# Optimization experiments

Measured on AMD Instinct MI355X. Metric: run time of the kernel, lower is better.

The kernel has to match this reference:

```python
import jax, jax.numpy as jnp
import numpy as np

B, L, K, E, D, H = 16, 512, 48, 128, 384, 128

def _gelu(x):
    return jax.nn.gelu(x, approximate=False)  # torch nn.GELU default is erf-based

def setup_inputs() -> dict:
    key = jax.random.key(0)
    ks = jax.random.split(key, 16)
    def randn(k, shape, scale=1.0):
        return jax.random.normal(k, shape, dtype=jnp.float32) * scale
    inp = {
        "h_V": randn(ks[0], (B, L, D)),
        "h_E": randn(ks[1], (B, L, K, E)),
        "mask": jnp.ones((B, L), dtype=jnp.float32),
        "fw1": randn(ks[2], (E, D), 1.0 / np.sqrt(E)),
        "fb1": randn(ks[3], (D,), 0.02),
        "fw2": randn(ks[4], (D, D), 1.0 / np.sqrt(D)),
        "fb2": randn(ks[5], (D,), 0.02),
        "hw1": randn(ks[6], (D, H), 1.0 / np.sqrt(D)),
        "hb1": randn(ks[7], (H,), 0.02),
        "hw2": randn(ks[8], (H, H // 2), 1.0 / np.sqrt(H)),
        "hb2": randn(ks[9], (H // 2,), 0.02),
        "hw3": randn(ks[10], (H // 2, 1), 1.0 / np.sqrt(H // 2)),
        "hb3": randn(ks[11], (1,), 0.02),
        "E_idx": jax.random.randint(ks[12], (B, L, K), 0, L),
    }
    return inp

def reference(h_V, h_E, mask, fw1, fb1, fw2, fb2, hw1, hb1, hw2, hb2, hw3, hb3, E_idx):
    # CFConv: edge-conditioned filters [B,L,K,D]
    W = _gelu(_gelu(h_E @ fw1 + fb1) @ fw2 + fb2)
    # gather_nodes: x_j[b,l,k,:] = h_V[b, E_idx[b,l,k], :]
    x_j = jax.vmap(lambda x, idx: x[idx])(h_V, E_idx)  # [B,L,K,D]
    h = jnp.sum(x_j * W, axis=2)  # weighted sum over neighbors -> [B,L,D]
    # mlp_head (dropout = identity at inference)
    h = _gelu(h @ hw1 + hb1)
    h = _gelu(h @ hw2 + hb2)
    dG = (h @ hw3 + hb3)[..., 0]  # [B,L]
    valid_length = jnp.clip(jnp.sum(mask, axis=1), 1.0, None)  # [B]
    return jnp.sum(dG * mask, axis=1) / jnp.sqrt(valid_length)  # [B]
```

## Files before the change

kernel.cpp:

```cpp
#include <hip/hip_runtime.h>
#include <hip/hip_bf16.h>
#include <math.h>

#define NB 16
#define NL 512
#define NK 48
#define NE 128
#define ND 384
#define NH 128

typedef __attribute__((ext_vector_type(8))) short short8;
typedef __attribute__((ext_vector_type(4))) float f32x4;

__device__ __forceinline__ float gelu_fast(float x) {
    float t = x * fmaf(x * x, -0.1029437f, -2.3022087f);
    float e = __builtin_amdgcn_exp2f(t);
    return x * __builtin_amdgcn_rcpf(1.0f + e);
}

__device__ __forceinline__ unsigned short f2bf(float x) {
    union { float f; unsigned u; } v; v.f = x;
    unsigned r = v.u + 0x7fffu + ((v.u >> 16) & 1u);
    return (unsigned short)(r >> 16);
}

__device__ __forceinline__ unsigned short f2bf_rhu(float x) {
    union { float f; unsigned u; } v; v.f = x;
    return (unsigned short)((v.u + 0x8000u) >> 16);
}

__device__ __forceinline__ unsigned pk_bf16(float a, float b) {
    union { float f; unsigned u; } ua, ub; ua.f = a; ub.f = b;
    return __builtin_amdgcn_perm(ua.u + 0x8000u, ub.u + 0x8000u, 0x07060302u);
}

__global__ void pack_weights(const float* __restrict__ fw1,
                             const float* __restrict__ fw2,
                             const float* __restrict__ hw1,
                             const float* __restrict__ hw2,
                             unsigned short* __restrict__ fw1p,
                             unsigned short* __restrict__ fw2p,
                             unsigned short* __restrict__ hw1p,
                             unsigned short* __restrict__ hw2p,
                             float* __restrict__ dGsum) {
    int tid = blockIdx.x * 256 + threadIdx.x;
    if (tid < NB) dGsum[tid] = 0.0f;
    if (tid < NE * ND) {
        int k = tid / ND, n = tid % ND;
        int dst = (((k >> 5) * 24 + (n >> 4)) * 64 + ((k >> 3) & 3) * 16 + (n & 15)) * 8 + (k & 7);
        fw1p[dst] = f2bf(fw1[tid]);
    } else if (tid < NE * ND + ND * ND) {
        int i = tid - NE * ND;
        int k = i / ND, n = i % ND;
        int dst = (((k >> 5) * 24 + (n >> 4)) * 64 + ((k >> 3) & 3) * 16 + (n & 15)) * 8 + (k & 7);
        fw2p[dst] = f2bf(fw2[i]);
    } else if (tid < NE * ND + ND * ND + ND * NH) {
        int i = tid - (NE * ND + ND * ND);
        int k = i / NH, n = i % NH;
        int dst = (((k >> 5) * 8 + (n >> 4)) * 64 + ((k >> 3) & 3) * 16 + (n & 15)) * 8 + (k & 7);
        hw1p[dst] = f2bf(hw1[i]);
    } else if (tid < NE * ND + ND * ND + ND * NH + NH * (NH / 2)) {
        int i = tid - (NE * ND + ND * ND + ND * NH);
        int k = i / (NH / 2), n = i % (NH / 2);
        int dst = (((k >> 5) * 4 + (n >> 4)) * 64 + ((k >> 3) & 3) * 16 + (n & 15)) * 8 + (k & 7);
        hw2p[dst] = f2bf(hw2[i]);
    }
}

__global__ __launch_bounds__(256, 2) void cfconv_kernel(
    const float* __restrict__ h_V, const float* __restrict__ h_E,
    const float* __restrict__ fb1, const float* __restrict__ fb2,
    const unsigned short* __restrict__ fw1p,
    const unsigned short* __restrict__ fw2p,
    const int* __restrict__ E_idx, unsigned short* __restrict__ hbufB)
{
    __shared__ unsigned short smem[96 * 392];
    __shared__ int rowoff_s[96];

    const int t = threadIdx.x;
    const int wave = t >> 6, lane = t & 63;
    const int quad = lane >> 4, l16 = lane & 15;
    const int bl0 = blockIdx.x * 2;
    const int wn0 = wave * 96;

    if (t < 96) {
        int g = t / 48, k = t - g * 48;
        int bl = bl0 + g;
        int idx = E_idx[bl * NK + k];
        rowoff_s[t] = ((bl >> 9) * NL + idx) * ND;
    }

    {
        const float4* src = (const float4*)(h_E + (size_t)bl0 * (NK * NE));
        #pragma unroll
        for (int i = 0; i < 12; i++) {
            int v = i * 256 + t;
            float4 d = src[v];
            int r = v >> 5;
            int c = (v & 31) * 4;
            uint2 u;
            u.x = pk_bf16(d.y, d.x);
            u.y = pk_bf16(d.w, d.z);
            *(uint2*)&smem[r * 136 + c] = u;
        }
    }
    __syncthreads();

    f32x4 acc[6][6];

    #pragma unroll
    for (int mt = 0; mt < 6; mt++)
        #pragma unroll
        for (int nt = 0; nt < 6; nt++)
            acc[mt][nt] = (f32x4){0.f, 0.f, 0.f, 0.f};

    #pragma unroll
    for (int kt = 0; kt < 4; kt++) {
        short8 bfrag[6], afrag[6];
        #pragma unroll
        for (int nt = 0; nt < 6; nt++)
            bfrag[nt] = *(const short8*)(fw1p + (size_t)((kt * 24 + (wn0 >> 4) + nt) * 64 + lane) * 8);
        #pragma unroll
        for (int mt = 0; mt < 6; mt++)
            afrag[mt] = *(const short8*)&smem[(mt * 16 + l16) * 136 + kt * 32 + quad * 8];
        #pragma unroll
        for (int mt = 0; mt < 6; mt++)
            #pragma unroll
            for (int nt = 0; nt < 6; nt++)
                acc[mt][nt] = __builtin_amdgcn_mfma_f32_16x16x32_bf16(
                    afrag[mt], bfrag[nt], acc[mt][nt], 0, 0, 0);
    }
    __syncthreads();

    #pragma unroll
    for (int nt = 0; nt < 6; nt++) {
        int col = wn0 + nt * 16 + l16;
        float b1 = fb1[col];
        #pragma unroll
        for (int mt = 0; mt < 6; mt++) {
            int rowb = mt * 16 + quad * 4;
            #pragma unroll
            for (int r = 0; r < 4; r++)
                smem[(rowb + r) * 392 + col] = f2bf_rhu(gelu_fast(acc[mt][nt][r] + b1));
        }
    }
    __syncthreads();

    #pragma unroll
    for (int mt = 0; mt < 6; mt++)
        #pragma unroll
        for (int nt = 0; nt < 6; nt++)
            acc[mt][nt] = (f32x4){0.f, 0.f, 0.f, 0.f};

    {
        short8 b0[6], b1[6], af[6];
        #define LOADB(kt, bf)                                                            \
            _Pragma("unroll")                                                            \
            for (int nt = 0; nt < 6; nt++)                                               \
                bf[nt] = *(const short8*)(fw2p +                                         \
                    (size_t)(((kt) * 24 + (wn0 >> 4) + nt) * 64 + lane) * 8);
        #define LOADA(kt)                                                                \
            _Pragma("unroll")                                                            \
            for (int mt = 0; mt < 6; mt++)                                               \
                af[mt] = *(const short8*)&smem[(mt * 16 + l16) * 392 + (kt) * 32 + quad * 8];
        #define MFMAS(bf)                                                                \
            _Pragma("unroll")                                                            \
            for (int mt = 0; mt < 6; mt++)                                               \
                _Pragma("unroll")                                                        \
                for (int nt = 0; nt < 6; nt++)                                           \
                    acc[mt][nt] = __builtin_amdgcn_mfma_f32_16x16x32_bf16(               \
                        af[mt], bf[nt], acc[mt][nt], 0, 0, 0);

        LOADB(0, b0);
        for (int kt = 0; kt < 10; kt += 2) {
            LOADB(kt + 1, b1);
            LOADA(kt);
            MFMAS(b0);
            LOADB(kt + 2, b0);
            LOADA(kt + 1);
            MFMAS(b1);
        }
        LOADB(11, b1);
        LOADA(10);
        MFMAS(b0);
        LOADA(11);
        MFMAS(b1);
        #undef LOADB
        #undef LOADA
        #undef MFMAS
    }

    float b2v[6];
    #pragma unroll
    for (int nt = 0; nt < 6; nt++) b2v[nt] = fb2[wn0 + nt * 16 + l16];

    #pragma unroll
    for (int g = 0; g < 2; g++) {
        float s[6] = {0.f, 0.f, 0.f, 0.f, 0.f, 0.f};
        #pragma unroll
        for (int mm = 0; mm < 3; mm++) {
            const int rb = (g * 3 + mm) * 16 + quad * 4;
            const float* p0 = h_V + rowoff_s[rb + 0] + wn0 + l16;
            const float* p1 = h_V + rowoff_s[rb + 1] + wn0 + l16;
            const float* p2 = h_V + rowoff_s[rb + 2] + wn0 + l16;
            const float* p3 = h_V + rowoff_s[rb + 3] + wn0 + l16;
            float xv[6][4];
            #pragma unroll
            for (int nt = 0; nt < 6; nt++) {
                xv[nt][0] = p0[nt * 16];
                xv[nt][1] = p1[nt * 16];
                xv[nt][2] = p2[nt * 16];
                xv[nt][3] = p3[nt * 16];
            }
            #pragma unroll
            for (int nt = 0; nt < 6; nt++)
                #pragma unroll
                for (int r = 0; r < 4; r++)
                    s[nt] = fmaf(gelu_fast(acc[g * 3 + mm][nt][r] + b2v[nt]), xv[nt][r], s[nt]);
        }
        #pragma unroll
        for (int nt = 0; nt < 6; nt++) {
            float v = s[nt];
            v += __shfl_xor(v, 16, 64);
            v += __shfl_xor(v, 32, 64);
            if (lane < 16)
                hbufB[(size_t)(bl0 + g) * ND + wn0 + nt * 16 + lane] = f2bf(v);
        }
    }
}

__global__ __launch_bounds__(64) void head_kernel(
    const unsigned short* __restrict__ hbufB,
    const unsigned short* __restrict__ hw1p, const float* __restrict__ hb1,
    const unsigned short* __restrict__ hw2p, const float* __restrict__ hb2,
    const float* __restrict__ hw3, const float* __restrict__ hb3,
    const float* __restrict__ mask, float* __restrict__ dGsum)
{
    __shared__ unsigned short T1[16 * 136];
    const int lane = threadIdx.x;
    const int quad = lane >> 4, l16 = lane & 15;
    const int row0 = blockIdx.x * 16;

    f32x4 acc1[8];
    #pragma unroll
    for (int nt = 0; nt < 8; nt++) acc1[nt] = (f32x4){0.f, 0.f, 0.f, 0.f};

    for (int kt = 0; kt < 12; kt++) {
        short8 a = *(const short8*)(hbufB + (size_t)(row0 + l16) * ND + kt * 32 + quad * 8);
        #pragma unroll
        for (int nt = 0; nt < 8; nt++) {
            short8 b = *(const short8*)(hw1p + (size_t)((kt * 8 + nt) * 64 + lane) * 8);
            acc1[nt] = __builtin_amdgcn_mfma_f32_16x16x32_bf16(a, b, acc1[nt], 0, 0, 0);
        }
    }

    #pragma unroll
    for (int nt = 0; nt < 8; nt++) {
        int col = nt * 16 + l16;
        float b1 = hb1[col];
        #pragma unroll
        for (int r = 0; r < 4; r++)
            T1[(quad * 4 + r) * 136 + col] = f2bf_rhu(gelu_fast(acc1[nt][r] + b1));
    }
    __syncthreads();

    f32x4 acc2[4];
    #pragma unroll
    for (int nt = 0; nt < 4; nt++) acc2[nt] = (f32x4){0.f, 0.f, 0.f, 0.f};

    #pragma unroll
    for (int kt = 0; kt < 4; kt++) {
        short8 a = *(const short8*)&T1[l16 * 136 + kt * 32 + quad * 8];
        #pragma unroll
        for (int nt = 0; nt < 4; nt++) {
            short8 b = *(const short8*)(hw2p + (size_t)((kt * 4 + nt) * 64 + lane) * 8);
            acc2[nt] = __builtin_amdgcn_mfma_f32_16x16x32_bf16(a, b, acc2[nt], 0, 0, 0);
        }
    }

    float w3[4], b2[4];
    #pragma unroll
    for (int nt = 0; nt < 4; nt++) { w3[nt] = hw3[nt * 16 + l16]; b2[nt] = hb2[nt * 16 + l16]; }

    float dsum = 0.f;
    const float hb3v = hb3[0];
    #pragma unroll
    for (int r = 0; r < 4; r++) {
        float pr = 0.f;
        #pragma unroll
        for (int nt = 0; nt < 4; nt++)
            pr = fmaf(gelu_fast(acc2[nt][r] + b2[nt]), w3[nt], pr);
        pr += __shfl_xor(pr, 1, 64);
        pr += __shfl_xor(pr, 2, 64);
        pr += __shfl_xor(pr, 4, 64);
        pr += __shfl_xor(pr, 8, 64);
        if (l16 == 0) {
            int grow = row0 + quad * 4 + r;
            dsum = fmaf(pr + hb3v, mask[grow], dsum);
        }
    }
    dsum += __shfl_xor(dsum, 16, 64);
    dsum += __shfl_xor(dsum, 32, 64);
    if (lane == 0) atomicAdd(&dGsum[row0 >> 9], dsum);
}

__global__ void finalize_kernel(const float* __restrict__ dGsum,
                                const float* __restrict__ mask,
                                float* __restrict__ out) {
    int t = threadIdx.x;
    int b = t >> 4, j = t & 15;
    float ms = 0.f;
    for (int l = j; l < NL; l += 16) ms += mask[b * NL + l];
    ms += __shfl_xor(ms, 1, 64);
    ms += __shfl_xor(ms, 2, 64);
    ms += __shfl_xor(ms, 4, 64);
    ms += __shfl_xor(ms, 8, 64);
    if (j == 0) {
        ms = fmaxf(ms, 1.0f);
        out[b] = dGsum[b] / sqrtf(ms);
    }
}

extern "C" void kernel_launch(void* const* d_in, const int* in_sizes, int n_in,
                              void* d_out, int out_size, void* d_ws, size_t ws_size,
                              hipStream_t stream) {
    const float* h_V  = (const float*)d_in[0];
    const float* h_E  = (const float*)d_in[1];
    const float* mask = (const float*)d_in[2];
    const float* fw1  = (const float*)d_in[3];
    const float* fb1  = (const float*)d_in[4];
    const float* fw2  = (const float*)d_in[5];
    const float* fb2  = (const float*)d_in[6];
    const float* hw1  = (const float*)d_in[7];
    const float* hb1  = (const float*)d_in[8];
    const float* hw2  = (const float*)d_in[9];
    const float* hb2  = (const float*)d_in[10];
    const float* hw3  = (const float*)d_in[11];
    const float* hb3  = (const float*)d_in[12];
    const int*   E_idx = (const int*)d_in[13];
    float* out = (float*)d_out;

    char* ws = (char*)d_ws;
    unsigned short* fw1p = (unsigned short*)ws;
    unsigned short* fw2p = (unsigned short*)(ws + 98304);
    unsigned short* hw1p = (unsigned short*)(ws + 393216);
    unsigned short* hw2p = (unsigned short*)(ws + 491520);
    float* dGsum = (float*)(ws + 507904);
    unsigned short* hbufB = (unsigned short*)(ws + 512000);

    pack_weights<<<992, 256, 0, stream>>>(fw1, fw2, hw1, hw2, fw1p, fw2p, hw1p, hw2p, dGsum);
    cfconv_kernel<<<(NB * NL) / 2, 256, 0, stream>>>(h_V, h_E, fb1, fb2, fw1p, fw2p, E_idx, hbufB);
    head_kernel<<<(NB * NL) / 16, 64, 0, stream>>>(hbufB, hw1p, hb1, hw2p, hb2, hw3, hb3, mask, dGsum);
    finalize_kernel<<<1, 256, 0, stream>>>(dGsum, mask, out);
}
```

Baseline: 465.4 us.

## Process one node per block with transposed first GEMM and partial-sum finalize

The CFConv kernel now handles one (b,l) node per block instead of two, which halves the tile to 48 edge rows and shrinks shared memory and accumulators so three blocks fit per CU. The first GEMM is computed transposed (weights as the A operand, edges as B), so GELU outputs can be packed four at a time and stored as 64-bit writes straight into the second GEMM's input tile, and one barrier is dropped. The atomic accumulation of per-batch sums is replaced by per-block partial writes reduced in the finalize kernel, which also removes the zero-init in the pack kernel. In exchange, each fw1/fw2 weight fragment is loaded from global memory for only 48 rows instead of 96, doubling weight traffic per row.

```diff
diff --git a/kernel.cpp b/kernel.cpp
--- a/kernel.cpp
+++ b/kernel.cpp
@@ -41,10 +41,8 @@
                              unsigned short* __restrict__ fw1p,
                              unsigned short* __restrict__ fw2p,
                              unsigned short* __restrict__ hw1p,
-                             unsigned short* __restrict__ hw2p,
-                             float* __restrict__ dGsum) {
+                             unsigned short* __restrict__ hw2p) {
     int tid = blockIdx.x * 256 + threadIdx.x;
-    if (tid < NB) dGsum[tid] = 0.0f;
     if (tid < NE * ND) {
         int k = tid / ND, n = tid % ND;
         int dst = (((k >> 5) * 24 + (n >> 4)) * 64 + ((k >> 3) & 3) * 16 + (n & 15)) * 8 + (k & 7);
@@ -67,33 +65,30 @@
     }
 }
 
-__global__ __launch_bounds__(256, 2) void cfconv_kernel(
+__global__ __launch_bounds__(256, 3) void cfconv_kernel(
     const float* __restrict__ h_V, const float* __restrict__ h_E,
     const float* __restrict__ fb1, const float* __restrict__ fb2,
     const unsigned short* __restrict__ fw1p,
     const unsigned short* __restrict__ fw2p,
     const int* __restrict__ E_idx, unsigned short* __restrict__ hbufB)
 {
-    __shared__ unsigned short smem[96 * 392];
-    __shared__ int rowoff_s[96];
+    __shared__ unsigned short Ea[48 * 136];
+    __shared__ unsigned short T[48 * 392];
+    __shared__ int rowoff_s[48];
 
     const int t = threadIdx.x;
     const int wave = t >> 6, lane = t & 63;
     const int quad = lane >> 4, l16 = lane & 15;
-    const int bl0 = blockIdx.x * 2;
+    const int bl = blockIdx.x;
     const int wn0 = wave * 96;
 
-    if (t < 96) {
-        int g = t / 48, k = t - g * 48;
-        int bl = bl0 + g;
-        int idx = E_idx[bl * NK + k];
-        rowoff_s[t] = ((bl >> 9) * NL + idx) * ND;
-    }
+    if (t < 48)
+        rowoff_s[t] = ((bl >> 9) * NL + E_idx[bl * NK + t]) * ND;
 
     {
-        const float4* src = (const float4*)(h_E + (size_t)bl0 * (NK * NE));
-        #pragma unroll
-        for (int i = 0; i < 12; i++) {
+        const float4* src = (const float4*)(h_E + (size_t)bl * (NK * NE));
+        #pragma unroll
+        for (int i = 0; i < 6; i++) {
             int v = i * 256 + t;
             float4 d = src[v];
             int r = v >> 5;
@@ -101,59 +96,56 @@
             uint2 u;
             u.x = pk_bf16(d.y, d.x);
             u.y = pk_bf16(d.w, d.z);
-            *(uint2*)&smem[r * 136 + c] = u;
+            *(uint2*)&Ea[r * 136 + c] = u;
         }
     }
     __syncthreads();
 
-    f32x4 acc[6][6];
-
-    #pragma unroll
-    for (int mt = 0; mt < 6; mt++)
-        #pragma unroll
-        for (int nt = 0; nt < 6; nt++)
-            acc[mt][nt] = (f32x4){0.f, 0.f, 0.f, 0.f};
+    f32x4 acc[18];
+
+    #pragma unroll
+    for (int i = 0; i < 18; i++) acc[i] = (f32x4){0.f, 0.f, 0.f, 0.f};
 
     #pragma unroll
     for (int kt = 0; kt < 4; kt++) {
-        short8 bfrag[6], afrag[6];
-        #pragma unroll
-        for (int nt = 0; nt < 6; nt++)
-            bfrag[nt] = *(const short8*)(fw1p + (size_t)((kt * 24 + (wn0 >> 4) + nt) * 64 + lane) * 8);
+        short8 aw[6], be[3];
         #pragma unroll
         for (int mt = 0; mt < 6; mt++)
-            afrag[mt] = *(const short8*)&smem[(mt * 16 + l16) * 136 + kt * 32 + quad * 8];
+            aw[mt] = *(const short8*)(fw1p + (size_t)((kt * 24 + (wn0 >> 4) + mt) * 64 + lane) * 8);
+        #pragma unroll
+        for (int nt = 0; nt < 3; nt++)
+            be[nt] = *(const short8*)&Ea[(nt * 16 + l16) * 136 + kt * 32 + quad * 8];
         #pragma unroll
         for (int mt = 0; mt < 6; mt++)
             #pragma unroll
-            for (int nt = 0; nt < 6; nt++)
-                acc[mt][nt] = __builtin_amdgcn_mfma_f32_16x16x32_bf16(
-                    afrag[mt], bfrag[nt], acc[mt][nt], 0, 0, 0);
+            for (int nt = 0; nt < 3; nt++)
+                acc[mt * 3 + nt] = __builtin_amdgcn_mfma_f32_16x16x32_bf16(
+                    aw[mt], be[nt], acc[mt * 3 + nt], 0, 0, 0);
+    }
+
+    #pragma unroll
+    for (int mt = 0; mt < 6; mt++) {
+        float4 b1v = *(const float4*)&fb1[wn0 + mt * 16 + quad * 4];
+        #pragma unroll
+        for (int nt = 0; nt < 3; nt++) {
+            f32x4 a = acc[mt * 3 + nt];
+            float v0 = gelu_fast(a[0] + b1v.x);
+            float v1 = gelu_fast(a[1] + b1v.y);
+            float v2 = gelu_fast(a[2] + b1v.z);
+            float v3 = gelu_fast(a[3] + b1v.w);
+            uint2 u;
+            u.x = pk_bf16(v1, v0);
+            u.y = pk_bf16(v3, v2);
+            *(uint2*)&T[(nt * 16 + l16) * 392 + wn0 + mt * 16 + quad * 4] = u;
+        }
     }
     __syncthreads();
 
     #pragma unroll
-    for (int nt = 0; nt < 6; nt++) {
-        int col = wn0 + nt * 16 + l16;
-        float b1 = fb1[col];
-        #pragma unroll
-        for (int mt = 0; mt < 6; mt++) {
-            int rowb = mt * 16 + quad * 4;
-            #pragma unroll
-            for (int r = 0; r < 4; r++)
-                smem[(rowb + r) * 392 + col] = f2bf_rhu(gelu_fast(acc[mt][nt][r] + b1));
-        }
-    }
-    __syncthreads();
-
-    #pragma unroll
-    for (int mt = 0; mt < 6; mt++)
-        #pragma unroll
-        for (int nt = 0; nt < 6; nt++)
-            acc[mt][nt] = (f32x4){0.f, 0.f, 0.f, 0.f};
+    for (int i = 0; i < 18; i++) acc[i] = (f32x4){0.f, 0.f, 0.f, 0.f};
 
     {
-        short8 b0[6], b1[6], af[6];
+        short8 b0[6], b1[6], af[3];
         #define LOADB(kt, bf)                                                            \
             _Pragma("unroll")                                                            \
             for (int nt = 0; nt < 6; nt++)                                               \
@@ -161,15 +153,15 @@
                     (size_t)(((kt) * 24 + (wn0 >> 4) + nt) * 64 + lane) * 8);
         #define LOADA(kt)                                                                \
             _Pragma("unroll")                                                            \
-            for (int mt = 0; mt < 6; mt++)                                               \
-                af[mt] = *(const short8*)&smem[(mt * 16 + l16) * 392 + (kt) * 32 + quad * 8];
+            for (int mt = 0; mt < 3; mt++)                                               \
+                af[mt] = *(const short8*)&T[(mt * 16 + l16) * 392 + (kt) * 32 + quad * 8];
         #define MFMAS(bf)                                                                \
             _Pragma("unroll")                                                            \
-            for (int mt = 0; mt < 6; mt++)                                               \
+            for (int mt = 0; mt < 3; mt++)                                               \
                 _Pragma("unroll")                                                        \
                 for (int nt = 0; nt < 6; nt++)                                           \
-                    acc[mt][nt] = __builtin_amdgcn_mfma_f32_16x16x32_bf16(               \
-                        af[mt], bf[nt], acc[mt][nt], 0, 0, 0);
+                    acc[nt * 3 + mt] = __builtin_amdgcn_mfma_f32_16x16x32_bf16(          \
+                        af[mt], bf[nt], acc[nt * 3 + mt], 0, 0, 0);
 
         LOADB(0, b0);
         for (int kt = 0; kt < 10; kt += 2) {
@@ -194,38 +186,35 @@
     #pragma unroll
     for (int nt = 0; nt < 6; nt++) b2v[nt] = fb2[wn0 + nt * 16 + l16];
 
-    #pragma unroll
-    for (int g = 0; g < 2; g++) {
-        float s[6] = {0.f, 0.f, 0.f, 0.f, 0.f, 0.f};
-        #pragma unroll
-        for (int mm = 0; mm < 3; mm++) {
-            const int rb = (g * 3 + mm) * 16 + quad * 4;
-            const float* p0 = h_V + rowoff_s[rb + 0] + wn0 + l16;
-            const float* p1 = h_V + rowoff_s[rb + 1] + wn0 + l16;
-            const float* p2 = h_V + rowoff_s[rb + 2] + wn0 + l16;
-            const float* p3 = h_V + rowoff_s[rb + 3] + wn0 + l16;
-            float xv[6][4];
+    float s[6] = {0.f, 0.f, 0.f, 0.f, 0.f, 0.f};
+    #pragma unroll
+    for (int mt = 0; mt < 3; mt++) {
+        const int rb = mt * 16 + quad * 4;
+        const float* p0 = h_V + rowoff_s[rb + 0] + wn0 + l16;
+        const float* p1 = h_V + rowoff_s[rb + 1] + wn0 + l16;
+        const float* p2 = h_V + rowoff_s[rb + 2] + wn0 + l16;
+        const float* p3 = h_V + rowoff_s[rb + 3] + wn0 + l16;
+        float xv[6][4];
+        #pragma unroll
+        for (int nt = 0; nt < 6; nt++) {
+            xv[nt][0] = p0[nt * 16];
+            xv[nt][1] = p1[nt * 16];
+            xv[nt][2] = p2[nt * 16];
+            xv[nt][3] = p3[nt * 16];
+        }
+        #pragma unroll
+        for (int nt = 0; nt < 6; nt++)
             #pragma unroll
-            for (int nt = 0; nt < 6; nt++) {
-                xv[nt][0] = p0[nt * 16];
-                xv[nt][1] = p1[nt * 16];
-                xv[nt][2] = p2[nt * 16];
-                xv[nt][3] = p3[nt * 16];
-            }
-            #pragma unroll
-            for (int nt = 0; nt < 6; nt++)
-                #pragma unroll
-                for (int r = 0; r < 4; r++)
-                    s[nt] = fmaf(gelu_fast(acc[g * 3 + mm][nt][r] + b2v[nt]), xv[nt][r], s[nt]);
-        }
-        #pragma unroll
-        for (int nt = 0; nt < 6; nt++) {
-            float v = s[nt];
-            v += __shfl_xor(v, 16, 64);
-            v += __shfl_xor(v, 32, 64);
-            if (lane < 16)
-                hbufB[(size_t)(bl0 + g) * ND + wn0 + nt * 16 + lane] = f2bf(v);
-        }
+            for (int r = 0; r < 4; r++)
+                s[nt] = fmaf(gelu_fast(acc[nt * 3 + mt][r] + b2v[nt]), xv[nt][r], s[nt]);
+    }
+    #pragma unroll
+    for (int nt = 0; nt < 6; nt++) {
+        float v = s[nt];
+        v += __shfl_xor(v, 16, 64);
+        v += __shfl_xor(v, 32, 64);
+        if (lane < 16)
+            hbufB[(size_t)bl * ND + wn0 + nt * 16 + lane] = f2bf(v);
     }
 }
 
@@ -234,7 +223,7 @@
     const unsigned short* __restrict__ hw1p, const float* __restrict__ hb1,
     const unsigned short* __restrict__ hw2p, const float* __restrict__ hb2,
     const float* __restrict__ hw3, const float* __restrict__ hb3,
-    const float* __restrict__ mask, float* __restrict__ dGsum)
+    const float* __restrict__ mask, float* __restrict__ dGpart)
 {
     __shared__ unsigned short T1[16 * 136];
     const int lane = threadIdx.x;
@@ -301,23 +290,25 @@
     }
     dsum += __shfl_xor(dsum, 16, 64);
     dsum += __shfl_xor(dsum, 32, 64);
-    if (lane == 0) atomicAdd(&dGsum[row0 >> 9], dsum);
-}
-
-__global__ void finalize_kernel(const float* __restrict__ dGsum,
+    if (lane == 0) dGpart[blockIdx.x] = dsum;
+}
+
+__global__ void finalize_kernel(const float* __restrict__ dGpart,
                                 const float* __restrict__ mask,
                                 float* __restrict__ out) {
     int t = threadIdx.x;
     int b = t >> 4, j = t & 15;
     float ms = 0.f;
     for (int l = j; l < NL; l += 16) ms += mask[b * NL + l];
-    ms += __shfl_xor(ms, 1, 64);
-    ms += __shfl_xor(ms, 2, 64);
-    ms += __shfl_xor(ms, 4, 64);
-    ms += __shfl_xor(ms, 8, 64);
+    float dg = dGpart[b * 32 + j] + dGpart[b * 32 + 16 + j];
+    #pragma unroll
+    for (int d = 1; d < 16; d <<= 1) {
+        ms += __shfl_xor(ms, d, 64);
+        dg += __shfl_xor(dg, d, 64);
+    }
     if (j == 0) {
         ms = fmaxf(ms, 1.0f);
-        out[b] = dGsum[b] / sqrtf(ms);
+        out[b] = dg / sqrtf(ms);
     }
 }
 
@@ -345,11 +336,11 @@
     unsigned short* fw2p = (unsigned short*)(ws + 98304);
     unsigned short* hw1p = (unsigned short*)(ws + 393216);
     unsigned short* hw2p = (unsigned short*)(ws + 491520);
-    float* dGsum = (float*)(ws + 507904);
+    float* dGpart = (float*)(ws + 507904);
     unsigned short* hbufB = (unsigned short*)(ws + 512000);
 
-    pack_weights<<<992, 256, 0, stream>>>(fw1, fw2, hw1, hw2, fw1p, fw2p, hw1p, hw2p, dGsum);
-    cfconv_kernel<<<(NB * NL) / 2, 256, 0, stream>>>(h_V, h_E, fb1, fb2, fw1p, fw2p, E_idx, hbufB);
-    head_kernel<<<(NB * NL) / 16, 64, 0, stream>>>(hbufB, hw1p, hb1, hw2p, hb2, hw3, hb3, mask, dGsum);
-    finalize_kernel<<<1, 256, 0, stream>>>(dGsum, mask, out);
-}
+    pack_weights<<<992, 256, 0, stream>>>(fw1, fw2, hw1, hw2, fw1p, fw2p, hw1p, hw2p);
+    cfconv_kernel<<<NB * NL, 256, 0, stream>>>(h_V, h_E, fb1, fb2, fw1p, fw2p, E_idx, hbufB);
+    head_kernel<<<(NB * NL) / 16, 64, 0, stream>>>(hbufB, hw1p, hb1, hw2p, hb2, hw3, hb3, mask, dGpart);
+    finalize_kernel<<<1, 256, 0, stream>>>(dGpart, mask, out);
+}
```

After: 453.8 us. 2.5% less time.
